# Kernel optimization log

Measured on AMD Instinct MI355X. Metric: run time of the kernel, lower is better.

## Reference

```python
import jax, jax.numpy as jnp
import numpy as np

R = 0.2          # stable-distribution hash bucket width
TABLE_SIZE = 2   # hash table size (buckets)
M = 5            # number of appended ALSH transform dims
EPS = 1e-12


def conv2d(x, W, b, pad):
    out = jax.lax.conv_general_dilated(
        x, W, window_strides=(1, 1), padding=[(pad, pad), (pad, pad)],
        dimension_numbers=('NCHW', 'OIHW', 'NCHW'))
    return out + b[None, :, None, None]


def maxpool2(x):
    return jax.lax.reduce_window(x, -jnp.inf, jax.lax.max,
                                 (1, 1, 2, 2), (1, 1, 2, 2), 'VALID')


def alsh_mask(x, W, a, c):
    """ALSH filter selection: hash P(kernels) and Q(query) with a stable
    distribution hash h(v)=floor((a.v+b)/r) mod table_size; active filters
    are those landing in the query's bucket. Returns [B, Cout] 0/1 mask.
    Multiplying conv output by this mask == gather active filters then
    zero_fill_missing back to full channel count."""
    Cout, Cin, kH, kW = W.shape
    Kf = W.reshape(Cout, -1)                       # [Cout, Cin*kH*kW]
    norms = jnp.linalg.norm(Kf, axis=1)
    Kn = Kf / (jnp.max(norms) + EPS)               # scale so all norms <= 1
    n = jnp.linalg.norm(Kn, axis=1, keepdims=True)
    # P transform: append norm^2, norm^4, ..., norm^(2^M)
    powers = jnp.concatenate([n ** (2 ** (i + 1)) for i in range(M)], axis=1)
    P = jnp.concatenate([Kn, powers], axis=1)      # [Cout, d+M]
    kh = jnp.mod(jnp.floor((P @ a + c[0]) / R), TABLE_SIZE)  # [Cout]
    # query vector: per-sample channel means broadcast over kernel support
    cm = x.mean(axis=(2, 3))                       # [B, Cin]
    q = jnp.repeat(cm, kH * kW, axis=1)            # [B, Cin*kH*kW] (cin,kh,kw order)
    qn = q / (jnp.linalg.norm(q, axis=1, keepdims=True) + EPS)
    # Q transform: append M halves
    Qv = jnp.concatenate([qn, jnp.full((q.shape[0], M), 0.5, q.dtype)], axis=1)
    qh = jnp.mod(jnp.floor((Qv @ a + c[0]) / R), TABLE_SIZE)  # [B]
    return (kh[None, :] == qh[:, None]).astype(x.dtype)       # [B, Cout]


def setup_inputs() -> dict:
    key = jax.random.key(0)
    ks = jax.random.split(key, 16)
    u = lambda k, s: jax.random.uniform(k, s, jnp.float32, 0.0, R)
    n = lambda k, s, sc=0.1: jax.random.normal(k, s, jnp.float32) * sc
    return {
        'x': jax.random.normal(ks[0], (4096, 3, 32, 32), jnp.float32),
        'W1': n(ks[1], (16, 3, 5, 5)), 'b1': n(ks[2], (16,)),
        'a1': jax.random.normal(ks[3], (80,), jnp.float32), 'c1': u(ks[4], (1,)),
        'W2': n(ks[5], (20, 16, 5, 5)), 'b2': n(ks[6], (20,)),
        'a2': jax.random.normal(ks[7], (405,), jnp.float32), 'c2': u(ks[8], (1,)),
        'W3': n(ks[9], (20, 20, 5, 5)), 'b3': n(ks[10], (20,)),
        'a3': jax.random.normal(ks[11], (505,), jnp.float32), 'c3': u(ks[12], (1,)),
        'Wo': n(ks[13], (10, 320)), 'bo': n(ks[14], (10,)),
    }


def reference(x, W1, b1, a1, c1, W2, b2, a2, c2, W3, b3, a3, c3, Wo, bo):
    m1 = alsh_mask(x, W1, a1, c1)
    h = jax.nn.relu(conv2d(x, W1, b1, 2)) * m1[:, :, None, None]
    h = maxpool2(h)                                # [B,16,16,16]
    m2 = alsh_mask(h, W2, a2, c2)
    h = jax.nn.relu(conv2d(h, W2, b2, 2)) * m2[:, :, None, None]
    h = maxpool2(h)                                # [B,20,8,8]
    m3 = alsh_mask(h, W3, a3, c3)
    h = jax.nn.relu(conv2d(h, W3, b3, 2)) * m3[:, :, None, None]
    # zero_fill_missing -> identity here: inactive channels already zero
    h = maxpool2(h)                                # [B,20,4,4]
    flat = h.reshape(h.shape[0], -1)               # [B,320]
    return flat @ Wo.T + bo
```

## Files before the change

kernel.cpp:

```cpp
#include <hip/hip_runtime.h>
#include <hip/hip_bf16.h>

#define EPSV 1e-12
#define RHASH 0.2

__device__ __forceinline__ int fmod2(double t) {
    return (int)(((long long)floor(t)) & 1LL);
}

__device__ __forceinline__ void load_row6(const float* base, float* r) {
    float2 a0 = *(const float2*)(base);
    float2 a1 = *(const float2*)(base + 2);
    float2 a2 = *(const float2*)(base + 4);
    r[0] = a0.x; r[1] = a0.y; r[2] = a1.x; r[3] = a1.y; r[4] = a2.x; r[5] = a2.y;
}

__device__ __forceinline__ void load_row12(const float* base, float* r) {
    #pragma unroll
    for (int j = 0; j < 6; ++j) *(float2*)&r[2 * j] = *(const float2*)(base + 2 * j);
}

#define FMA4(c,kx,w) { float wg=(w); \
  acc[c][0]=fmaf(wg,cur[kx],acc[c][0]); acc[c][1]=fmaf(wg,cur[(kx)+1],acc[c][1]); \
  acc[c][2]=fmaf(wg,nxt[kx],acc[c][2]); acc[c][3]=fmaf(wg,nxt[(kx)+1],acc[c][3]); }

__device__ void layer_setup(const float* W, const float* a, double cval,
                            int Co, int Ci, int* kh, double* asum, double* qc,
                            double* s_norm, float* Wbuf, float* abuf)
{
    const int t = threadIdx.x;
    const int D = Ci * 25;
    for (int i = t; i < Co * D; i += 256) Wbuf[i] = W[i];
    for (int i = t; i < D + 5; i += 256) abuf[i] = a[i];
    __syncthreads();
    if (t < Co) {
        double s = 0;
        for (int j = 0; j < D; ++j) { double w = (double)Wbuf[t * D + j]; s += w * w; }
        s_norm[t] = sqrt(s);
    }
    __syncthreads();
    if (t == 0) {
        double mx = 0;
        for (int i = 0; i < Co; ++i) mx = fmax(mx, s_norm[i]);
        s_norm[23] = 1.0 / (mx + EPSV);
    }
    __syncthreads();
    double scale = s_norm[23];
    if (t < Co) {
        double dp = 0;
        for (int j = 0; j < D; ++j) dp += (double)Wbuf[t * D + j] * (double)abuf[j];
        dp *= scale;
        double n = s_norm[t] * scale;
        double p = n * n;
        for (int m = 0; m < 5; ++m) { dp += p * (double)abuf[D + m]; p *= p; }
        kh[t] = fmod2((dp + cval) / RHASH);
    }
    if (t >= 64 && t < 64 + Ci) {
        int c = t - 64;
        double s = 0;
        for (int j = 0; j < 25; ++j) s += (double)abuf[c * 25 + j];
        asum[c] = s;
    }
    if (t == 128) {
        double s = 0;
        for (int m = 0; m < 5; ++m) s += (double)abuf[D + m];
        *qc = 0.5 * s + cval;
    }
    __syncthreads();
}

__global__ __launch_bounds__(256) void prep_kernel(
    const float* W1, const float* a1, const float* c1,
    const float* W2, const float* a2, const float* c2,
    const float* W3, const float* a3, const float* c3,
    double* dmeta, int* imeta,
    float* Wp1, float* Wp2, float* Wp3)
{
    __shared__ float Wbuf[10000];
    __shared__ float abuf[512];
    __shared__ double s_norm[24];
    const int blk = blockIdx.x;
    if (blk == 0) {
        layer_setup(W1, a1, (double)c1[0], 16, 3,  imeta + 0,  dmeta + 0,  dmeta + 39, s_norm, Wbuf, abuf);
    } else if (blk == 1) {
        layer_setup(W2, a2, (double)c2[0], 20, 16, imeta + 16, dmeta + 3,  dmeta + 40, s_norm, Wbuf, abuf);
    } else if (blk == 2) {
        layer_setup(W3, a3, (double)c3[0], 20, 20, imeta + 36, dmeta + 19, dmeta + 41, s_norm, Wbuf, abuf);
    } else {
        int i = (blk - 3) * 256 + threadIdx.x;
        if (i < 1200) {
            int co = i & 15, r = i >> 4;
            int kx = r % 5, r2 = r / 5, ky = r2 % 5, ci = r2 / 5;
            Wp1[i] = W1[co * 75 + ci * 25 + ky * 5 + kx];
        } else if (i < 1200 + 8960) {
            int k = i - 1200;
            int j = k % 28, r = k / 28;
            int cog = r % 4, r2 = r / 4, ky = r2 % 5, ci = r2 / 5;
            Wp2[k] = (j < 25) ? W2[(cog * 5 + j / 5) * 400 + ci * 25 + ky * 5 + (j % 5)] : 0.f;
        } else if (i < 1200 + 8960 + 11200) {
            int k = i - 10160;
            int j = k % 28, r = k / 28;
            int cog = r % 4, r2 = r / 4, ky = r2 % 5, ci = r2 / 5;
            Wp3[k] = (j < 25) ? W3[(cog * 5 + j / 5) * 500 + ci * 25 + ky * 5 + (j % 5)] : 0.f;
        }
    }
}

__global__ __launch_bounds__(256) void conv1_kernel(
    const float* __restrict__ x, const float* __restrict__ Wp1,
    const float* __restrict__ b1, const int* __restrict__ kh1,
    const double* __restrict__ dmeta, float* __restrict__ h1,
    int* __restrict__ qh2)
{
    __shared__ float xs[3][36][38];
    __shared__ float Ws[1200];
    __shared__ double s_red[3];
    __shared__ double s_ch[16][4];

    const int b = blockIdx.x, t = threadIdx.x;
    const int w = t >> 6, ln = t & 63;

    for (int i = t; i < 3 * 36 * 38; i += 256) (&xs[0][0][0])[i] = 0.f;
    for (int i = t; i < 600; i += 256) ((float2*)Ws)[i] = ((const float2*)Wp1)[i];
    __syncthreads();
    const float2* xb2 = (const float2*)(x + (size_t)b * 3072);
    for (int i = t; i < 1536; i += 256) {
        int c = i >> 9, rem = i & 511;
        int row = rem >> 4, col2 = rem & 15;
        *(float2*)&xs[c][row + 2][col2 * 2 + 2] = xb2[i];
    }
    __syncthreads();

    if (w < 3) {
        double s = 0;
        for (int j = 0; j < 16; ++j) {
            int i = ln + 64 * j;
            s += (double)xs[w][(i >> 5) + 2][(i & 31) + 2];
        }
        #pragma unroll
        for (int off = 32; off; off >>= 1) s += __shfl_xor(s, off);
        if (ln == 0) s_red[w] = s;
    }
    __syncthreads();
    double dp = 0, nn = 0;
    #pragma unroll
    for (int c = 0; c < 3; ++c) {
        double cm = s_red[c] * (1.0 / 1024.0);
        dp += cm * dmeta[c]; nn += cm * cm;
    }
    const int qh = fmod2((dp / (5.0 * sqrt(nn) + EPSV) + dmeta[39]) / RHASH);

    const int cog = ln >> 4;
    const int py = 4 * w + ((ln >> 2) & 3), pxg = ln & 3;
    const int y0 = 2 * py, x0 = 8 * pxg;

    float accA[4][8], accB[4][8];
    #pragma unroll
    for (int c = 0; c < 4; ++c) {
        float bb = b1[cog * 4 + c];
        #pragma unroll
        for (int k = 0; k < 8; ++k) { accA[c][k] = bb; accB[c][k] = bb; }
    }

    #pragma unroll
    for (int ci = 0; ci < 3; ++ci) {
        float ra[12], rb[12];
        load_row12(&xs[ci][y0][x0],     ra);
        load_row12(&xs[ci][y0 + 1][x0], rb);
        #pragma unroll
        for (int ky = 0; ky < 5; ++ky) {
            const float4* wq = (const float4*)&Ws[((ci * 5 + ky) * 5) * 16 + cog * 4];
            #pragma unroll
            for (int kx = 0; kx < 5; ++kx) {
                float4 wv = wq[kx * 4];
                { float wg = wv.x;
                  #pragma unroll
                  for (int k = 0; k < 8; ++k) { accA[0][k] = fmaf(wg, ra[k + kx], accA[0][k]);
                                                accB[0][k] = fmaf(wg, rb[k + kx], accB[0][k]); } }
                { float wg = wv.y;
                  #pragma unroll
                  for (int k = 0; k < 8; ++k) { accA[1][k] = fmaf(wg, ra[k + kx], accA[1][k]);
                                                accB[1][k] = fmaf(wg, rb[k + kx], accB[1][k]); } }
                { float wg = wv.z;
                  #pragma unroll
                  for (int k = 0; k < 8; ++k) { accA[2][k] = fmaf(wg, ra[k + kx], accA[2][k]);
                                                accB[2][k] = fmaf(wg, rb[k + kx], accB[2][k]); } }
                { float wg = wv.w;
                  #pragma unroll
                  for (int k = 0; k < 8; ++k) { accA[3][k] = fmaf(wg, ra[k + kx], accA[3][k]);
                                                accB[3][k] = fmaf(wg, rb[k + kx], accB[3][k]); } }
            }
            if (ky < 4) {
                #pragma unroll
                for (int j = 0; j < 12; ++j) ra[j] = rb[j];
                load_row12(&xs[ci][y0 + ky + 2][x0], rb);
            }
        }
    }

    float* hb = h1 + (size_t)b * 4096 + py * 16 + pxg * 4;
    double csum[4];
    #pragma unroll
    for (int c = 0; c < 4; ++c) {
        int co = cog * 4 + c;
        float mask = (kh1[co] == qh) ? 1.f : 0.f;
        float v0 = fmaxf(fmaxf(accA[c][0], accA[c][1]), fmaxf(accB[c][0], accB[c][1]));
        float v1 = fmaxf(fmaxf(accA[c][2], accA[c][3]), fmaxf(accB[c][2], accB[c][3]));
        float v2 = fmaxf(fmaxf(accA[c][4], accA[c][5]), fmaxf(accB[c][4], accB[c][5]));
        float v3 = fmaxf(fmaxf(accA[c][6], accA[c][7]), fmaxf(accB[c][6], accB[c][7]));
        v0 = fmaxf(v0, 0.f) * mask; v1 = fmaxf(v1, 0.f) * mask;
        v2 = fmaxf(v2, 0.f) * mask; v3 = fmaxf(v3, 0.f) * mask;
        *(float4*)(hb + co * 256) = make_float4(v0, v1, v2, v3);
        csum[c] = (double)v0 + (double)v1 + (double)v2 + (double)v3;
    }
    #pragma unroll
    for (int c = 0; c < 4; ++c) {
        double s = csum[c];
        s += __shfl_xor(s, 8); s += __shfl_xor(s, 4);
        s += __shfl_xor(s, 2); s += __shfl_xor(s, 1);
        if ((ln & 15) == 0) s_ch[cog * 4 + c][w] = s;
    }
    __syncthreads();
    if (t == 0) {
        double dp2 = 0, nn2 = 0;
        #pragma unroll
        for (int c = 0; c < 16; ++c) {
            double cm = (s_ch[c][0] + s_ch[c][1] + s_ch[c][2] + s_ch[c][3]) * (1.0 / 256.0);
            dp2 += cm * dmeta[3 + c]; nn2 += cm * cm;
        }
        qh2[b] = fmod2((dp2 / (5.0 * sqrt(nn2) + EPSV) + dmeta[40]) / RHASH);
    }
}

#define C2_XLOAD(CH, RX) { \
    _Pragma("unroll") \
    for (int j = 0; j < 8; ++j) { \
        int i = t + 256 * j, si = i >> 9, rem = i & 511, cil = rem >> 7, rr = rem & 127; \
        RX[j] = (b0 + si < B) ? ((const float2*)h1)[(size_t)(b0 + si) * 2048 + ((CH) * 4 + cil) * 128 + rr] \
                              : make_float2(0.f, 0.f); \
    } }

#define C2_XCOMMIT(RX) { \
    _Pragma("unroll") \
    for (int j = 0; j < 8; ++j) { \
        int i = t + 256 * j, si = i >> 9, rem = i & 511, cil = rem >> 7, rr = rem & 127; \
        int p2 = rr * 2, row = p2 >> 4, col = p2 & 15; \
        *(float2*)&xs[si][cil][row + 2][col + 2] = RX[j]; \
    } }

__global__ __launch_bounds__(256) void conv2_kernel(
    const float* __restrict__ h1, const float* __restrict__ Wp2,
    const float* __restrict__ b2, const int* __restrict__ kh2,
    const int* __restrict__ qh2, const double* __restrict__ dmeta,
    float* __restrict__ h2, int* __restrict__ qh3, int B)
{
    __shared__ float xs[4][4][20][22];
    __shared__ float Ws[2240];
    __shared__ double s_ch[4][20];

    const int b0 = blockIdx.x * 4, t = threadIdx.x;
    const int s = t >> 6, l = t & 63;
    const int cog = l >> 4, pos = l & 15;
    const int py = pos >> 1, pxg = pos & 1;
    const int b = b0 + s;

    for (int i = t; i < 4 * 4 * 20 * 22; i += 256) (&xs[0][0][0][0])[i] = 0.f;

    const int qh = (b < B) ? qh2[b] : 0;
    float accA[5][8], accB[5][8];
    #pragma unroll
    for (int c = 0; c < 5; ++c) {
        float bb = b2[cog * 5 + c];
        #pragma unroll
        for (int k = 0; k < 8; ++k) { accA[c][k] = bb; accB[c][k] = bb; }
    }

    float2 rx[8];
    C2_XLOAD(0, rx);

    for (int ch = 0; ch < 4; ++ch) {
        for (int i = t; i < 1120; i += 256)
            ((float2*)Ws)[i] = ((const float2*)(Wp2 + ch * 2240))[i];
        C2_XCOMMIT(rx);
        __syncthreads();
        if (ch < 3) C2_XLOAD(ch + 1, rx);

        for (int cil = 0; cil < 4; ++cil) {
            float ra[12], rb[12];
            load_row12(&xs[s][cil][2 * py][8 * pxg],     ra);
            load_row12(&xs[s][cil][2 * py + 1][8 * pxg], rb);
            #pragma unroll
            for (int ky = 0; ky < 5; ++ky) {
                float wv[28];
                const float4* wp = (const float4*)&Ws[((cil * 5 + ky) * 4 + cog) * 28];
                *(float4*)&wv[0]  = wp[0];
                *(float4*)&wv[4]  = wp[1];
                *(float4*)&wv[8]  = wp[2];
                *(float4*)&wv[12] = wp[3];
                *(float4*)&wv[16] = wp[4];
                *(float4*)&wv[20] = wp[5];
                *(float4*)&wv[24] = wp[6];
                #pragma unroll
                for (int c = 0; c < 5; ++c) {
                    #pragma unroll
                    for (int kx = 0; kx < 5; ++kx) {
                        float wg = wv[c * 5 + kx];
                        #pragma unroll
                        for (int k = 0; k < 8; ++k) {
                            accA[c][k] = fmaf(wg, ra[k + kx], accA[c][k]);
                            accB[c][k] = fmaf(wg, rb[k + kx], accB[c][k]);
                        }
                    }
                }
                if (ky < 4) {
                    #pragma unroll
                    for (int j = 0; j < 12; ++j) ra[j] = rb[j];
                    load_row12(&xs[s][cil][2 * py + ky + 2][8 * pxg], rb);
                }
            }
        }
        __syncthreads();
    }

    float* ob = h2 + (size_t)b * 1280 + py * 8 + pxg * 4;
    double csum[5];
    #pragma unroll
    for (int c = 0; c < 5; ++c) {
        int co = cog * 5 + c;
        float mask = (kh2[co] == qh) ? 1.f : 0.f;
        float v0 = fmaxf(fmaxf(accA[c][0], accA[c][1]), fmaxf(accB[c][0], accB[c][1]));
        float v1 = fmaxf(fmaxf(accA[c][2], accA[c][3]), fmaxf(accB[c][2], accB[c][3]));
        float v2 = fmaxf(fmaxf(accA[c][4], accA[c][5]), fmaxf(accB[c][4], accB[c][5]));
        float v3 = fmaxf(fmaxf(accA[c][6], accA[c][7]), fmaxf(accB[c][6], accB[c][7]));
        v0 = fmaxf(v0, 0.f) * mask; v1 = fmaxf(v1, 0.f) * mask;
        v2 = fmaxf(v2, 0.f) * mask; v3 = fmaxf(v3, 0.f) * mask;
        if (b < B) *(float4*)(ob + co * 64) = make_float4(v0, v1, v2, v3);
        csum[c] = (double)v0 + (double)v1 + (double)v2 + (double)v3;
    }
    #pragma unroll
    for (int c = 0; c < 5; ++c) {
        double sv = csum[c];
        sv += __shfl_xor(sv, 8); sv += __shfl_xor(sv, 4);
        sv += __shfl_xor(sv, 2); sv += __shfl_xor(sv, 1);
        if (pos == 0) s_ch[s][cog * 5 + c] = sv;
    }
    __syncthreads();
    if (l == 0 && b < B) {
        double dp2 = 0, nn2 = 0;
        #pragma unroll
        for (int c = 0; c < 20; ++c) {
            double cm = s_ch[s][c] * (1.0 / 64.0);
            dp2 += cm * dmeta[19 + c]; nn2 += cm * cm;
        }
        qh3[b] = fmod2((dp2 / (5.0 * sqrt(nn2) + EPSV) + dmeta[41]) / RHASH);
    }
}

#define C3_WLOAD(CH, RW) { \
    _Pragma("unroll") \
    for (int j = 0; j < 6; ++j) { \
        int i = t + 256 * j; \
        if (i < 1400) RW[j] = ((const float2*)(Wp3 + (CH) * 2800))[i]; \
    } }

#define C3_WCOMMIT(RW) { \
    _Pragma("unroll") \
    for (int j = 0; j < 6; ++j) { \
        int i = t + 256 * j; \
        if (i < 1400) ((float2*)Ws)[i] = RW[j]; \
    } }

#define C3_XLOAD(CH, RX) { \
    _Pragma("unroll") \
    for (int j = 0; j < 3; ++j) { \
        int i = t + 256 * j; \
        if (i < 640) { \
            int ss = i / 160, r = i - ss * 160, ci = r >> 5, rr = r & 31; \
            RX[j] = (b0 + ss < B) ? ((const float2*)(h2 + (size_t)(b0 + ss) * 1280 + ((CH) * 5 + ci) * 64))[rr] \
                                  : make_float2(0.f, 0.f); \
        } \
    } }

#define C3_XCOMMIT(RX) { \
    _Pragma("unroll") \
    for (int j = 0; j < 3; ++j) { \
        int i = t + 256 * j; \
        if (i < 640) { \
            int ss = i / 160, r = i - ss * 160, ci = r >> 5, rr = r & 31, p2 = rr * 2; \
            *(float2*)&xs[ss][ci][(p2 >> 3) + 2][(p2 & 7) + 2] = RX[j]; \
        } \
    } }

__global__ __launch_bounds__(256) void conv3_kernel(
    const float* __restrict__ h2, const float* __restrict__ Wp3,
    const float* __restrict__ b3, const int* __restrict__ kh3,
    const int* __restrict__ qh3,
    const float* __restrict__ Wo, const float* __restrict__ bo,
    float* __restrict__ out, int B)
{
    __shared__ float xs[4][5][12][12];
    __shared__ float Ws[2800];
    __shared__ float flat[4][320];

    const int b0 = blockIdx.x * 4, t = threadIdx.x;
    const int s = t >> 6, q0 = t & 63, cog = q0 >> 4, pos = q0 & 15;
    const int py = pos >> 2, px = pos & 3;
    const int y0 = 2 * py, x0 = 2 * px;
    const int b = b0 + s;

    for (int i = t; i < 4 * 5 * 144; i += 256) (&xs[0][0][0][0])[i] = 0.f;

    const int qh = (b < B) ? qh3[b] : 0;
    float acc[5][4];
    #pragma unroll
    for (int c = 0; c < 5; ++c) {
        float bb = b3[cog * 5 + c];
        acc[c][0] = bb; acc[c][1] = bb; acc[c][2] = bb; acc[c][3] = bb;
    }

    float2 rw[6], rx[3];
    C3_WLOAD(0, rw);
    C3_XLOAD(0, rx);

    for (int ch = 0; ch < 4; ++ch) {
        C3_WCOMMIT(rw);
        C3_XCOMMIT(rx);
        __syncthreads();
        if (ch < 3) { C3_WLOAD(ch + 1, rw); C3_XLOAD(ch + 1, rx); }

        #pragma unroll
        for (int ci = 0; ci < 5; ++ci) {
            float cur[6], nxt[6];
            load_row6(&xs[s][ci][y0][x0], cur);
            load_row6(&xs[s][ci][y0 + 1][x0], nxt);
            #pragma unroll
            for (int ky = 0; ky < 5; ++ky) {
                const float* wrow = &Ws[((ci * 5 + ky) * 4 + cog) * 28];
                const float4* wq = (const float4*)wrow;
                float4 q;
                q = wq[0]; FMA4(0, 0, q.x) FMA4(0, 1, q.y) FMA4(0, 2, q.z) FMA4(0, 3, q.w)
                q = wq[1]; FMA4(0, 4, q.x) FMA4(1, 0, q.y) FMA4(1, 1, q.z) FMA4(1, 2, q.w)
                q = wq[2]; FMA4(1, 3, q.x) FMA4(1, 4, q.y) FMA4(2, 0, q.z) FMA4(2, 1, q.w)
                q = wq[3]; FMA4(2, 2, q.x) FMA4(2, 3, q.y) FMA4(2, 4, q.z) FMA4(3, 0, q.w)
                q = wq[4]; FMA4(3, 1, q.x) FMA4(3, 2, q.y) FMA4(3, 3, q.z) FMA4(3, 4, q.w)
                q = wq[5]; FMA4(4, 0, q.x) FMA4(4, 1, q.y) FMA4(4, 2, q.z) FMA4(4, 3, q.w)
                FMA4(4, 4, wrow[24])
                if (ky < 4) {
                    #pragma unroll
                    for (int j = 0; j < 6; ++j) cur[j] = nxt[j];
                    load_row6(&xs[s][ci][y0 + ky + 2][x0], nxt);
                }
            }
        }
        __syncthreads();
    }

    #pragma unroll
    for (int c = 0; c < 5; ++c) {
        int co = cog * 5 + c;
        float m = fmaxf(fmaxf(acc[c][0], acc[c][1]), fmaxf(acc[c][2], acc[c][3]));
        flat[s][co * 16 + pos] = fmaxf(m, 0.f) * ((kh3[co] == qh) ? 1.f : 0.f);
    }
    __syncthreads();

    if (t < 160) {
        const int g = t >> 2, qq = t & 3;
        const int ss = g / 10, o = g - ss * 10;
        float a = 0.f;
        const float* wr = Wo + o * 320;
        for (int k = qq; k < 320; k += 4) a = fmaf(flat[ss][k], wr[k], a);
        a += __shfl_xor(a, 1);
        a += __shfl_xor(a, 2);
        if (qq == 0 && b0 + ss < B) out[(size_t)(b0 + ss) * 10 + o] = a + bo[o];
    }
}

extern "C" void kernel_launch(void* const* d_in, const int* in_sizes, int n_in,
                              void* d_out, int out_size, void* d_ws, size_t ws_size,
                              hipStream_t stream)
{
    const float* x  = (const float*)d_in[0];
    const float* W1 = (const float*)d_in[1];
    const float* b1 = (const float*)d_in[2];
    const float* a1 = (const float*)d_in[3];
    const float* c1 = (const float*)d_in[4];
    const float* W2 = (const float*)d_in[5];
    const float* b2 = (const float*)d_in[6];
    const float* a2 = (const float*)d_in[7];
    const float* c2 = (const float*)d_in[8];
    const float* W3 = (const float*)d_in[9];
    const float* b3 = (const float*)d_in[10];
    const float* a3 = (const float*)d_in[11];
    const float* c3 = (const float*)d_in[12];
    const float* Wo = (const float*)d_in[13];
    const float* bo = (const float*)d_in[14];
    float* out = (float*)d_out;

    const int B = in_sizes[0] / 3072;

    float* h1  = (float*)d_ws;
    float* h2  = h1 + (size_t)B * 4096;
    float* Wp1 = h2 + (size_t)B * 1280;
    float* Wp2 = Wp1 + 1200;
    float* Wp3 = Wp2 + 8960;
    double* dmeta = (double*)(Wp3 + 11200);
    int* imeta = (int*)(dmeta + 42);
    int* qh2 = imeta + 56;
    int* qh3 = qh2 + B;

    prep_kernel<<<87, 256, 0, stream>>>(W1, a1, c1, W2, a2, c2, W3, a3, c3,
                                        dmeta, imeta, Wp1, Wp2, Wp3);
    conv1_kernel<<<B, 256, 0, stream>>>(x, Wp1, b1, imeta, dmeta, h1, qh2);
    conv2_kernel<<<(B + 3) / 4, 256, 0, stream>>>(h1, Wp2, b2, imeta + 16, qh2, dmeta, h2, qh3, B);
    conv3_kernel<<<(B + 3) / 4, 256, 0, stream>>>(h2, Wp3, b3, imeta + 36, qh3, Wo, bo, out, B);
}
```

Baseline: 487.3 us.

## Fuse conv2 and conv3+FC into one kernel keeping h2 in shared memory

Merges the conv2 and conv3 kernels into one. The pooled conv2 output stays in a reused shared-memory buffer with padded rows, so the h2 global write and re-read are gone, along with one launch. The conv3 weights are now staged in ten smaller chunks with extra barriers, padding rows are handled through a zero-row pointer, and the final FC becomes a per-wave shuffle reduction. The trade-off is more synchronisation and a serial conv3 weight load that is no longer prefetched.

```diff
diff --git a/kernel.cpp b/kernel.cpp
--- a/kernel.cpp
+++ b/kernel.cpp
@@ -232,6 +232,8 @@
     }
 }
 
+#define XSP(si,ci,row,col) (u + (((si) * 4 + (ci)) * 20 + (row)) * 22 + (col))
+
 #define C2_XLOAD(CH, RX) { \
     _Pragma("unroll") \
     for (int j = 0; j < 8; ++j) { \
@@ -245,28 +247,34 @@
     for (int j = 0; j < 8; ++j) { \
         int i = t + 256 * j, si = i >> 9, rem = i & 511, cil = rem >> 7, rr = rem & 127; \
         int p2 = rr * 2, row = p2 >> 4, col = p2 & 15; \
-        *(float2*)&xs[si][cil][row + 2][col + 2] = RX[j]; \
+        *(float2*)XSP(si, cil, row + 2, col + 2) = RX[j]; \
     } }
 
-__global__ __launch_bounds__(256) void conv2_kernel(
+__global__ __launch_bounds__(256) void conv23_kernel(
     const float* __restrict__ h1, const float* __restrict__ Wp2,
-    const float* __restrict__ b2, const int* __restrict__ kh2,
-    const int* __restrict__ qh2, const double* __restrict__ dmeta,
-    float* __restrict__ h2, int* __restrict__ qh3, int B)
+    const float* __restrict__ b2, const float* __restrict__ b3,
+    const int* __restrict__ imeta, const int* __restrict__ qh2,
+    const double* __restrict__ dmeta, const float* __restrict__ Wp3,
+    const float* __restrict__ Wo, const float* __restrict__ bo,
+    float* __restrict__ out, int B)
 {
-    __shared__ float xs[4][4][20][22];
-    __shared__ float Ws[2240];
+    __shared__ float u[9280];
     __shared__ double s_ch[4][20];
+    __shared__ int s_qh[4];
 
     const int b0 = blockIdx.x * 4, t = threadIdx.x;
     const int s = t >> 6, l = t & 63;
     const int cog = l >> 4, pos = l & 15;
-    const int py = pos >> 1, pxg = pos & 1;
     const int b = b0 + s;
-
-    for (int i = t; i < 4 * 4 * 20 * 22; i += 256) (&xs[0][0][0][0])[i] = 0.f;
-
-    const int qh = (b < B) ? qh2[b] : 0;
+    const bool valid = (b < B);
+
+    const int py2 = pos >> 1, pxg = pos & 1;
+    float* Ws2 = u + 7040;
+    const int* kh2 = imeta + 16;
+
+    for (int i = t; i < 7040; i += 256) u[i] = 0.f;
+
+    const int qh = valid ? qh2[b] : 0;
     float accA[5][8], accB[5][8];
     #pragma unroll
     for (int c = 0; c < 5; ++c) {
@@ -277,22 +285,23 @@
 
     float2 rx[8];
     C2_XLOAD(0, rx);
+    __syncthreads();
 
     for (int ch = 0; ch < 4; ++ch) {
         for (int i = t; i < 1120; i += 256)
-            ((float2*)Ws)[i] = ((const float2*)(Wp2 + ch * 2240))[i];
+            ((float2*)Ws2)[i] = ((const float2*)(Wp2 + ch * 2240))[i];
         C2_XCOMMIT(rx);
         __syncthreads();
         if (ch < 3) C2_XLOAD(ch + 1, rx);
 
         for (int cil = 0; cil < 4; ++cil) {
             float ra[12], rb[12];
-            load_row12(&xs[s][cil][2 * py][8 * pxg],     ra);
-            load_row12(&xs[s][cil][2 * py + 1][8 * pxg], rb);
+            load_row12(XSP(s, cil, 2 * py2, 8 * pxg),     ra);
+            load_row12(XSP(s, cil, 2 * py2 + 1, 8 * pxg), rb);
             #pragma unroll
             for (int ky = 0; ky < 5; ++ky) {
                 float wv[28];
-                const float4* wp = (const float4*)&Ws[((cil * 5 + ky) * 4 + cog) * 28];
+                const float4* wp = (const float4*)&Ws2[((cil * 5 + ky) * 4 + cog) * 28];
                 *(float4*)&wv[0]  = wp[0];
                 *(float4*)&wv[4]  = wp[1];
                 *(float4*)&wv[8]  = wp[2];
@@ -315,14 +324,22 @@
                 if (ky < 4) {
                     #pragma unroll
                     for (int j = 0; j < 12; ++j) ra[j] = rb[j];
-                    load_row12(&xs[s][cil][2 * py + ky + 2][8 * pxg], rb);
+                    load_row12(XSP(s, cil, 2 * py2 + ky + 2, 8 * pxg), rb);
                 }
             }
         }
         __syncthreads();
     }
 
-    float* ob = h2 + (size_t)b * 1280 + py * 8 + pxg * 4;
+    float* h2s  = u;
+    float* zrow = u + 8800;
+
+    for (int i = t; i < 2560; i += 256) {
+        int r = i >> 2, hc = i & 3;
+        u[r * 12 + ((hc < 2) ? hc : hc + 8)] = 0.f;
+    }
+    if (t < 12) zrow[t] = 0.f;
+
     double csum[5];
     #pragma unroll
     for (int c = 0; c < 5; ++c) {
@@ -334,7 +351,9 @@
         float v3 = fmaxf(fmaxf(accA[c][6], accA[c][7]), fmaxf(accB[c][6], accB[c][7]));
         v0 = fmaxf(v0, 0.f) * mask; v1 = fmaxf(v1, 0.f) * mask;
         v2 = fmaxf(v2, 0.f) * mask; v3 = fmaxf(v3, 0.f) * mask;
-        if (b < B) *(float4*)(ob + co * 64) = make_float4(v0, v1, v2, v3);
+        int base = ((s * 20 + co) * 8 + py2) * 12 + 2 + pxg * 4;
+        *(float2*)&u[base]     = make_float2(v0, v1);
+        *(float2*)&u[base + 2] = make_float2(v2, v3);
         csum[c] = (double)v0 + (double)v1 + (double)v2 + (double)v3;
     }
     #pragma unroll
@@ -345,72 +364,22 @@
         if (pos == 0) s_ch[s][cog * 5 + c] = sv;
     }
     __syncthreads();
-    if (l == 0 && b < B) {
+    if (l == 0) {
         double dp2 = 0, nn2 = 0;
         #pragma unroll
         for (int c = 0; c < 20; ++c) {
             double cm = s_ch[s][c] * (1.0 / 64.0);
             dp2 += cm * dmeta[19 + c]; nn2 += cm * cm;
         }
-        qh3[b] = fmod2((dp2 / (5.0 * sqrt(nn2) + EPSV) + dmeta[41]) / RHASH);
-    }
-}
-
-#define C3_WLOAD(CH, RW) { \
-    _Pragma("unroll") \
-    for (int j = 0; j < 6; ++j) { \
-        int i = t + 256 * j; \
-        if (i < 1400) RW[j] = ((const float2*)(Wp3 + (CH) * 2800))[i]; \
-    } }
-
-#define C3_WCOMMIT(RW) { \
-    _Pragma("unroll") \
-    for (int j = 0; j < 6; ++j) { \
-        int i = t + 256 * j; \
-        if (i < 1400) ((float2*)Ws)[i] = RW[j]; \
-    } }
-
-#define C3_XLOAD(CH, RX) { \
-    _Pragma("unroll") \
-    for (int j = 0; j < 3; ++j) { \
-        int i = t + 256 * j; \
-        if (i < 640) { \
-            int ss = i / 160, r = i - ss * 160, ci = r >> 5, rr = r & 31; \
-            RX[j] = (b0 + ss < B) ? ((const float2*)(h2 + (size_t)(b0 + ss) * 1280 + ((CH) * 5 + ci) * 64))[rr] \
-                                  : make_float2(0.f, 0.f); \
-        } \
-    } }
-
-#define C3_XCOMMIT(RX) { \
-    _Pragma("unroll") \
-    for (int j = 0; j < 3; ++j) { \
-        int i = t + 256 * j; \
-        if (i < 640) { \
-            int ss = i / 160, r = i - ss * 160, ci = r >> 5, rr = r & 31, p2 = rr * 2; \
-            *(float2*)&xs[ss][ci][(p2 >> 3) + 2][(p2 & 7) + 2] = RX[j]; \
-        } \
-    } }
-
-__global__ __launch_bounds__(256) void conv3_kernel(
-    const float* __restrict__ h2, const float* __restrict__ Wp3,
-    const float* __restrict__ b3, const int* __restrict__ kh3,
-    const int* __restrict__ qh3,
-    const float* __restrict__ Wo, const float* __restrict__ bo,
-    float* __restrict__ out, int B)
-{
-    __shared__ float xs[4][5][12][12];
-    __shared__ float Ws[2800];
-    __shared__ float flat[4][320];
-
-    const int b0 = blockIdx.x * 4, t = threadIdx.x;
-    const int s = t >> 6, q0 = t & 63, cog = q0 >> 4, pos = q0 & 15;
-    const int py = pos >> 2, px = pos & 3;
-    const int y0 = 2 * py, x0 = 2 * px;
-    const int b = b0 + s;
-
-    for (int i = t; i < 4 * 5 * 144; i += 256) (&xs[0][0][0][0])[i] = 0.f;
-
-    const int qh = (b < B) ? qh3[b] : 0;
+        s_qh[s] = fmod2((dp2 / (5.0 * sqrt(nn2) + EPSV) + dmeta[41]) / RHASH);
+    }
+
+    const int* kh3 = imeta + 36;
+    const int py3 = pos >> 2, px3 = pos & 3;
+    const int r0 = 2 * py3 - 2;
+    const int x0 = 2 * px3;
+    float* Ws3 = u + 7680;
+
     float acc[5][4];
     #pragma unroll
     for (int c = 0; c < 5; ++c) {
@@ -418,24 +387,24 @@
         acc[c][0] = bb; acc[c][1] = bb; acc[c][2] = bb; acc[c][3] = bb;
     }
 
-    float2 rw[6], rx[3];
-    C3_WLOAD(0, rw);
-    C3_XLOAD(0, rx);
-
-    for (int ch = 0; ch < 4; ++ch) {
-        C3_WCOMMIT(rw);
-        C3_XCOMMIT(rx);
+    for (int ch = 0; ch < 10; ++ch) {
         __syncthreads();
-        if (ch < 3) { C3_WLOAD(ch + 1, rw); C3_XLOAD(ch + 1, rx); }
-
-        #pragma unroll
-        for (int ci = 0; ci < 5; ++ci) {
+        for (int i = t; i < 560; i += 256)
+            ((float2*)Ws3)[i] = ((const float2*)(Wp3 + ch * 1120))[i];
+        __syncthreads();
+
+        #pragma unroll
+        for (int ci2 = 0; ci2 < 2; ++ci2) {
+            const int ci = ch * 2 + ci2;
+            const float* rb0 = u + ((s * 20 + ci) * 8) * 12 + x0;
             float cur[6], nxt[6];
-            load_row6(&xs[s][ci][y0][x0], cur);
-            load_row6(&xs[s][ci][y0 + 1][x0], nxt);
+            { const float* p = (r0 >= 0 && r0 < 8) ? (rb0 + r0 * 12) : zrow;
+              load_row6(p, cur); }
+            { int r = r0 + 1; const float* p = (r >= 0 && r < 8) ? (rb0 + r * 12) : zrow;
+              load_row6(p, nxt); }
             #pragma unroll
             for (int ky = 0; ky < 5; ++ky) {
-                const float* wrow = &Ws[((ci * 5 + ky) * 4 + cog) * 28];
+                const float* wrow = &Ws3[((ci2 * 5 + ky) * 4 + cog) * 28];
                 const float4* wq = (const float4*)wrow;
                 float4 q;
                 q = wq[0]; FMA4(0, 0, q.x) FMA4(0, 1, q.y) FMA4(0, 2, q.z) FMA4(0, 3, q.w)
@@ -448,30 +417,30 @@
                 if (ky < 4) {
                     #pragma unroll
                     for (int j = 0; j < 6; ++j) cur[j] = nxt[j];
-                    load_row6(&xs[s][ci][y0 + ky + 2][x0], nxt);
+                    int r = r0 + ky + 2;
+                    const float* p = (r >= 0 && r < 8) ? (rb0 + r * 12) : zrow;
+                    load_row6(p, nxt);
                 }
             }
         }
-        __syncthreads();
-    }
-
+    }
+
+    const int qh3v = s_qh[s];
+    float pv[5];
     #pragma unroll
     for (int c = 0; c < 5; ++c) {
-        int co = cog * 5 + c;
         float m = fmaxf(fmaxf(acc[c][0], acc[c][1]), fmaxf(acc[c][2], acc[c][3]));
-        flat[s][co * 16 + pos] = fmaxf(m, 0.f) * ((kh3[co] == qh) ? 1.f : 0.f);
-    }
-    __syncthreads();
-
-    if (t < 160) {
-        const int g = t >> 2, qq = t & 3;
-        const int ss = g / 10, o = g - ss * 10;
-        float a = 0.f;
-        const float* wr = Wo + o * 320;
-        for (int k = qq; k < 320; k += 4) a = fmaf(flat[ss][k], wr[k], a);
-        a += __shfl_xor(a, 1);
-        a += __shfl_xor(a, 2);
-        if (qq == 0 && b0 + ss < B) out[(size_t)(b0 + ss) * 10 + o] = a + bo[o];
+        pv[c] = fmaxf(m, 0.f) * ((kh3[cog * 5 + c] == qh3v) ? 1.f : 0.f);
+    }
+    #pragma unroll
+    for (int o = 0; o < 10; ++o) {
+        float p = 0.f;
+        #pragma unroll
+        for (int c = 0; c < 5; ++c)
+            p = fmaf(pv[c], Wo[o * 320 + (cog * 5 + c) * 16 + pos], p);
+        p += __shfl_xor(p, 32); p += __shfl_xor(p, 16); p += __shfl_xor(p, 8);
+        p += __shfl_xor(p, 4);  p += __shfl_xor(p, 2);  p += __shfl_xor(p, 1);
+        if (l == 0 && valid) out[(size_t)b * 10 + o] = p + bo[o];
     }
 }
 
@@ -506,11 +475,10 @@
     double* dmeta = (double*)(Wp3 + 11200);
     int* imeta = (int*)(dmeta + 42);
     int* qh2 = imeta + 56;
-    int* qh3 = qh2 + B;
 
     prep_kernel<<<87, 256, 0, stream>>>(W1, a1, c1, W2, a2, c2, W3, a3, c3,
                                         dmeta, imeta, Wp1, Wp2, Wp3);
     conv1_kernel<<<B, 256, 0, stream>>>(x, Wp1, b1, imeta, dmeta, h1, qh2);
-    conv2_kernel<<<(B + 3) / 4, 256, 0, stream>>>(h1, Wp2, b2, imeta + 16, qh2, dmeta, h2, qh3, B);
-    conv3_kernel<<<(B + 3) / 4, 256, 0, stream>>>(h2, Wp3, b3, imeta + 36, qh3, Wo, bo, out, B);
-}
+    conv23_kernel<<<(B + 3) / 4, 256, 0, stream>>>(h1, Wp2, b2, b3, imeta, qh2,
+                                                   dmeta, Wp3, Wo, bo, out, B);
+}
```

Result: slower. 530.1 us (+8.8%).
